# Optimization experiments

Hardware: AMD Instinct MI355X
Metric: run time of the kernel (lower is better)

Reference implementation:

```python
import jax, jax.numpy as jnp
import numpy as np

B, A, EMBED, HIDDEN, PROJ = 256, 16, 1024, 1024, 256


def setup_inputs() -> dict:
    key = jax.random.key(0)
    k0, k1, k2 = jax.random.split(key, 3)
    return {
        "agent_embeddings": jax.random.normal(k0, (B, A, EMBED), dtype=jnp.float32),
        "w1": jax.random.normal(k1, (EMBED, HIDDEN), dtype=jnp.float32) * (1.0 / np.sqrt(EMBED)),
        "b1": jnp.zeros((HIDDEN,), dtype=jnp.float32),
        "w2": jax.random.normal(k2, (HIDDEN, PROJ), dtype=jnp.float32) * (1.0 / np.sqrt(HIDDEN)),
        "b2": jnp.zeros((PROJ,), dtype=jnp.float32),
        "log_scale": jnp.asarray(0.0, dtype=jnp.float32),  # log(init_logit_scale=1.0)
        "logit_bias": jnp.asarray(0.0, dtype=jnp.float32),
    }


def reference(agent_embeddings, w1, b1, w2, b2, log_scale, logit_bias):
    b, a, d = agent_embeddings.shape
    n = b * a
    x = agent_embeddings.reshape(n, d)
    # MLP projector: Linear -> GELU (exact, torch default) -> [dropout=identity at eval] -> Linear
    h = jax.nn.gelu(x @ w1 + b1, approximate=False)
    p = h @ w2 + b2  # [N, proj_dim]
    z = p / jnp.linalg.norm(p, axis=-1, keepdims=True)
    # cosine similarity logits, scaled + biased
    logits = (z @ z.T) * jnp.exp(log_scale) + logit_bias  # [N, N]
    # block-diagonal labels: 1 iff same batch element
    ids = jnp.arange(n) // a
    m1 = jnp.where(ids[:, None] == ids[None, :], 1.0, -1.0)  # 2*labels - 1
    loglik = jax.nn.log_sigmoid(m1 * logits)
    loss = jnp.mean(-jnp.sum(loglik, axis=-1))
    embeddings = z.reshape(b, a, -1)
    return embeddings, loss, logits
```

## Files before the change

### kernel.cpp

```cpp
#include <hip/hip_runtime.h>
#include <math.h>


#define NTOK 4096
#define DEMB 1024
#define DHID 1024
#define DPRJ 256

typedef __attribute__((ext_vector_type(8))) short bf16x8;
typedef __attribute__((ext_vector_type(4))) float f32x4;

typedef __attribute__((address_space(3))) void lds_void_t;
typedef __attribute__((address_space(1))) const void gbl_void_t;

static __device__ __forceinline__ void glds16(const void* g, void* l) {
    __builtin_amdgcn_global_load_lds((gbl_void_t*)g, (lds_void_t*)l, 16, 0, 0);
}

static __device__ __forceinline__ void split2(float v, ushort* h, ushort* l) {
    const uint u = __float_as_uint(v);
    *h = (ushort)(u >> 16);
    const float r = v - __uint_as_float(u & 0xffff0000u);
    *l = (ushort)(__float_as_uint(r) >> 16);
}
static __device__ __forceinline__ float gelu_fast(float v) {
    const float x  = v * 0.70710678118654752440f;
    const float ax = fabsf(x);
    const float t  = 1.0f / (1.0f + 0.3275911f * ax);
    const float poly = t * (0.254829592f + t * (-0.284496736f + t * (1.421413741f
                     + t * (-1.453152027f + t * 1.061405429f))));
    const float erf_ax = 1.0f - poly * __expf(-ax * ax);
    return 0.5f * v * (1.0f + copysignf(erf_ax, x));
}
static __device__ __forceinline__ float log_sigmoid_fast(float x) {
    return fminf(x, 0.0f) - __logf(1.0f + __expf(-fabsf(x)));
}

__global__ __launch_bounds__(256)
void k_cvt_T(const float* __restrict__ W, ushort* __restrict__ WtH,
             ushort* __restrict__ WtL, int K, int N)
{
    __shared__ float tile[32][33];
    const int tn0 = blockIdx.x * 32;
    const int tk0 = blockIdx.y * 32;
    const int tr = threadIdx.x >> 5;
    const int tc = threadIdx.x & 31;
#pragma unroll
    for (int p = 0; p < 4; ++p)
        tile[tr + 8 * p][tc] = W[(size_t)(tk0 + tr + 8 * p) * N + tn0 + tc];
    __syncthreads();
#pragma unroll
    for (int p = 0; p < 4; ++p) {
        const int n = tr + 8 * p;
        ushort h, l;
        split2(tile[tc][n], &h, &l);
        WtH[(size_t)(tn0 + n) * K + tk0 + tc] = h;
        WtL[(size_t)(tn0 + n) * K + tk0 + tc] = l;
    }
}

#define G1_BUF 12288
__global__ __launch_bounds__(256, 3)
void k_gemm1(const float* __restrict__ X,
             const ushort* __restrict__ W1tH, const ushort* __restrict__ W1tL,
             const float* __restrict__ B1,
             ushort* __restrict__ Hh, ushort* __restrict__ Hl)
{
    __shared__ __align__(16) ushort sm[2 * G1_BUF];
    const int t = threadIdx.x, lane = t & 63, w = t >> 6;
    const int wr = w >> 1, wc = w & 1;
    const int bm = blockIdx.x * 128, bn = blockIdx.y * 64;
    const int kb = lane >> 4, lr = lane & 15;

    const int ar = t & 63;
    const float* xp0 = X + (size_t)(bm + ar) * DEMB + w * 8;
    const float* xp1 = xp0 + (size_t)64 * DEMB;
    const ushort* bhs = W1tH + (size_t)(bn + lane) * DEMB + w * 8;
    const ushort* bls = W1tL + (size_t)(bn + lane) * DEMB + w * 8;

    f32x4 acc[4][2];
#pragma unroll
    for (int i = 0; i < 4; ++i)
#pragma unroll
        for (int j = 0; j < 2; ++j) acc[i][j] = (f32x4){0.f, 0.f, 0.f, 0.f};

    {
        const float4 a00 = *(const float4*)(xp0);
        const float4 a01 = *(const float4*)(xp0 + 4);
        const float4 a10 = *(const float4*)(xp1);
        const float4 a11 = *(const float4*)(xp1 + 4);
        glds16(bhs, sm + 8192 + w * 512);
        glds16(bls, sm + 10240 + w * 512);
        const float va[8] = {a00.x, a00.y, a00.z, a00.w, a01.x, a01.y, a01.z, a01.w};
        const float vb[8] = {a10.x, a10.y, a10.z, a10.w, a11.x, a11.y, a11.z, a11.w};
        uint4 h0, l0, h1, l1;
#pragma unroll
        for (int e = 0; e < 8; ++e) {
            split2(va[e], (ushort*)&h0 + e, (ushort*)&l0 + e);
            split2(vb[e], (ushort*)&h1 + e, (ushort*)&l1 + e);
        }
        *(uint4*)(sm + w * 1024 + ar * 8)               = h0;
        *(uint4*)(sm + 4096 + w * 1024 + ar * 8)        = l0;
        *(uint4*)(sm + w * 1024 + (ar + 64) * 8)        = h1;
        *(uint4*)(sm + 4096 + w * 1024 + (ar + 64) * 8) = l1;
        __syncthreads();
    }

    int co = 0;
#pragma unroll 2
    for (int ks = 0; ks < 32; ++ks) {
        float4 a00, a01, a10, a11;
        if (ks < 31) {
            const int kt = (ks + 1) * 32;
            a00 = *(const float4*)(xp0 + kt);
            a01 = *(const float4*)(xp0 + kt + 4);
            a10 = *(const float4*)(xp1 + kt);
            a11 = *(const float4*)(xp1 + kt + 4);
            ushort* nb = sm + (co ^ G1_BUF);
            glds16(bhs + kt, nb + 8192 + w * 512);
            glds16(bls + kt, nb + 10240 + w * 512);
        }
        const ushort* cb = sm + co;
        bf16x8 bh[2], bl[2];
#pragma unroll
        for (int j = 0; j < 2; ++j) {
            const int o = kb * 512 + (wc * 32 + j * 16 + lr) * 8;
            bh[j] = *(const bf16x8*)(cb + 8192 + o);
            bl[j] = *(const bf16x8*)(cb + 10240 + o);
        }
#pragma unroll
        for (int i = 0; i < 4; ++i) {
            const int o = kb * 1024 + (wr * 64 + i * 16 + lr) * 8;
            const bf16x8 ah = *(const bf16x8*)(cb + o);
            const bf16x8 al = *(const bf16x8*)(cb + 4096 + o);
#pragma unroll
            for (int j = 0; j < 2; ++j) {
                acc[i][j] = __builtin_amdgcn_mfma_f32_16x16x32_bf16(ah, bh[j], acc[i][j], 0, 0, 0);
                acc[i][j] = __builtin_amdgcn_mfma_f32_16x16x32_bf16(ah, bl[j], acc[i][j], 0, 0, 0);
                acc[i][j] = __builtin_amdgcn_mfma_f32_16x16x32_bf16(al, bh[j], acc[i][j], 0, 0, 0);
            }
        }
        if (ks < 31) {
            ushort* nb = sm + (co ^ G1_BUF);
            const float va[8] = {a00.x, a00.y, a00.z, a00.w, a01.x, a01.y, a01.z, a01.w};
            const float vb[8] = {a10.x, a10.y, a10.z, a10.w, a11.x, a11.y, a11.z, a11.w};
            uint4 h0, l0, h1, l1;
#pragma unroll
            for (int e = 0; e < 8; ++e) {
                split2(va[e], (ushort*)&h0 + e, (ushort*)&l0 + e);
                split2(vb[e], (ushort*)&h1 + e, (ushort*)&l1 + e);
            }
            *(uint4*)(nb + w * 1024 + ar * 8)               = h0;
            *(uint4*)(nb + 4096 + w * 1024 + ar * 8)        = l0;
            *(uint4*)(nb + w * 1024 + (ar + 64) * 8)        = h1;
            *(uint4*)(nb + 4096 + w * 1024 + (ar + 64) * 8) = l1;
        }
        __syncthreads();
        co ^= G1_BUF;
    }

#pragma unroll
    for (int j = 0; j < 2; ++j) {
        const int col = bn + wc * 32 + j * 16 + lr;
        const float b = B1[col];
#pragma unroll
        for (int i = 0; i < 4; ++i) {
#pragma unroll
            for (int e = 0; e < 4; ++e) {
                const int row = bm + wr * 64 + i * 16 + kb * 4 + e;
                const float g = gelu_fast(acc[i][j][e] + b);
                ushort h, l;
                split2(g, &h, &l);
                Hh[(size_t)row * DHID + col] = h;
                Hl[(size_t)row * DHID + col] = l;
            }
        }
    }
}

#define G2_BUF 12288
__global__ __launch_bounds__(256, 3)
void k_gemm2(const ushort* __restrict__ Hh, const ushort* __restrict__ Hl,
             const ushort* __restrict__ W2tH, const ushort* __restrict__ W2tL,
             float* __restrict__ P)
{
    __shared__ __align__(16) ushort sm[2 * G2_BUF];
    const int t = threadIdx.x, lane = t & 63, w = t >> 6;
    const int wr = w >> 1, wc = w & 1;
    const int bm = blockIdx.x * 128, bn = blockIdx.y * 64;
    const int k0 = blockIdx.z * 512;
    const int kb = lane >> 4, lr = lane & 15;

    const ushort* ah0 = Hh + (size_t)(bm + lane) * DHID + k0 + w * 8;
    const ushort* ah1 = Hh + (size_t)(bm + 64 + lane) * DHID + k0 + w * 8;
    const ushort* al0 = Hl + (size_t)(bm + lane) * DHID + k0 + w * 8;
    const ushort* al1 = Hl + (size_t)(bm + 64 + lane) * DHID + k0 + w * 8;
    const ushort* bhs = W2tH + (size_t)(bn + lane) * DHID + k0 + w * 8;
    const ushort* bls = W2tL + (size_t)(bn + lane) * DHID + k0 + w * 8;

    f32x4 acc[4][2];
#pragma unroll
    for (int i = 0; i < 4; ++i)
#pragma unroll
        for (int j = 0; j < 2; ++j) acc[i][j] = (f32x4){0.f, 0.f, 0.f, 0.f};

#define G2_STAGE(buf, kt)                                   \
    glds16(ah0 + (kt), (buf) + w * 1024);                   \
    glds16(ah1 + (kt), (buf) + w * 1024 + 512);             \
    glds16(al0 + (kt), (buf) + 4096 + w * 1024);            \
    glds16(al1 + (kt), (buf) + 4096 + w * 1024 + 512);      \
    glds16(bhs + (kt), (buf) + 8192 + w * 512);             \
    glds16(bls + (kt), (buf) + 10240 + w * 512);

    { G2_STAGE(sm, 0); __syncthreads(); }

    int co = 0;
#pragma unroll 2
    for (int ks = 0; ks < 16; ++ks) {
        if (ks < 15) {
            ushort* nb = sm + (co ^ G2_BUF);
            const int kt = (ks + 1) * 32;
            G2_STAGE(nb, kt);
        }
        const ushort* cb = sm + co;
        bf16x8 bh[2], bl[2];
#pragma unroll
        for (int j = 0; j < 2; ++j) {
            const int o = kb * 512 + (wc * 32 + j * 16 + lr) * 8;
            bh[j] = *(const bf16x8*)(cb + 8192 + o);
            bl[j] = *(const bf16x8*)(cb + 10240 + o);
        }
#pragma unroll
        for (int i = 0; i < 4; ++i) {
            const int o = kb * 1024 + (wr * 64 + i * 16 + lr) * 8;
            const bf16x8 ah = *(const bf16x8*)(cb + o);
            const bf16x8 al = *(const bf16x8*)(cb + 4096 + o);
#pragma unroll
            for (int j = 0; j < 2; ++j) {
                acc[i][j] = __builtin_amdgcn_mfma_f32_16x16x32_bf16(ah, bh[j], acc[i][j], 0, 0, 0);
                acc[i][j] = __builtin_amdgcn_mfma_f32_16x16x32_bf16(ah, bl[j], acc[i][j], 0, 0, 0);
                acc[i][j] = __builtin_amdgcn_mfma_f32_16x16x32_bf16(al, bh[j], acc[i][j], 0, 0, 0);
            }
        }
        __syncthreads();
        co ^= G2_BUF;
    }

    float* Pz = P + (size_t)blockIdx.z * NTOK * DPRJ;
#pragma unroll
    for (int j = 0; j < 2; ++j) {
        const int col = bn + wc * 32 + j * 16 + lr;
#pragma unroll
        for (int i = 0; i < 4; ++i) {
#pragma unroll
            for (int e = 0; e < 4; ++e) {
                const int row = bm + wr * 64 + i * 16 + kb * 4 + e;
                Pz[(size_t)row * DPRJ + col] = acc[i][j][e];
            }
        }
    }
}

__global__ __launch_bounds__(256)
void k_norm(const float* __restrict__ P, const float* __restrict__ B2,
            float* __restrict__ Zo, ushort* __restrict__ Zbh,
            ushort* __restrict__ Zbl)
{
    const int r = blockIdx.x;
    const int c = threadIdx.x;

    const float v = P[(size_t)r * DPRJ + c]
                  + P[(size_t)NTOK * DPRJ + (size_t)r * DPRJ + c] + B2[c];
    float ss = v * v;
#pragma unroll
    for (int o = 32; o > 0; o >>= 1) ss += __shfl_down(ss, o);
    __shared__ float wsum[4];
    if ((c & 63) == 0) wsum[c >> 6] = ss;
    __syncthreads();
    const float tot = wsum[0] + wsum[1] + wsum[2] + wsum[3];
    const float z = v / sqrtf(tot);
    Zo[(size_t)r * DPRJ + c] = z;
    ushort h, l;
    split2(z, &h, &l);
    Zbh[(size_t)r * DPRJ + c] = h;
    Zbl[(size_t)r * DPRJ + c] = l;
}

#define G3_BUF 16384
__global__ __launch_bounds__(256, 2)
void k_gemm3(const ushort* __restrict__ Zbh, const ushort* __restrict__ Zbl,
             const float* __restrict__ LS, const float* __restrict__ LB,
             float* __restrict__ Lg, float* __restrict__ partial)
{
    __shared__ __align__(16) ushort sm[2 * G3_BUF];
    const int t = threadIdx.x, lane = t & 63, w = t >> 6;
    const int wr = w >> 1, wc = w & 1;
    const int bm = blockIdx.x * 128, bn = blockIdx.y * 128;
    const int kb = lane >> 4, lr = lane & 15;

    const ushort* aH0 = Zbh + (size_t)(bm + lane) * DPRJ + w * 8;
    const ushort* aH1 = Zbh + (size_t)(bm + 64 + lane) * DPRJ + w * 8;
    const ushort* aL0 = Zbl + (size_t)(bm + lane) * DPRJ + w * 8;
    const ushort* aL1 = Zbl + (size_t)(bm + 64 + lane) * DPRJ + w * 8;
    const ushort* bH0 = Zbh + (size_t)(bn + lane) * DPRJ + w * 8;
    const ushort* bH1 = Zbh + (size_t)(bn + 64 + lane) * DPRJ + w * 8;
    const ushort* bL0 = Zbl + (size_t)(bn + lane) * DPRJ + w * 8;
    const ushort* bL1 = Zbl + (size_t)(bn + 64 + lane) * DPRJ + w * 8;

    f32x4 acc[4][4];
#pragma unroll
    for (int i = 0; i < 4; ++i)
#pragma unroll
        for (int j = 0; j < 4; ++j) acc[i][j] = (f32x4){0.f, 0.f, 0.f, 0.f};

#define G3_STAGE(buf, kt)                                    \
    glds16(aH0 + (kt), (buf) + w * 1024);                    \
    glds16(aH1 + (kt), (buf) + w * 1024 + 512);              \
    glds16(aL0 + (kt), (buf) + 4096 + w * 1024);             \
    glds16(aL1 + (kt), (buf) + 4096 + w * 1024 + 512);       \
    glds16(bH0 + (kt), (buf) + 8192 + w * 1024);             \
    glds16(bH1 + (kt), (buf) + 8192 + w * 1024 + 512);       \
    glds16(bL0 + (kt), (buf) + 12288 + w * 1024);            \
    glds16(bL1 + (kt), (buf) + 12288 + w * 1024 + 512);

    { G3_STAGE(sm, 0); __syncthreads(); }

    int co = 0;
#pragma unroll
    for (int ks = 0; ks < 8; ++ks) {
        if (ks < 7) {
            ushort* nb = sm + (co ^ G3_BUF);
            const int kt = (ks + 1) * 32;
            G3_STAGE(nb, kt);
        }
        const ushort* cb = sm + co;
        bf16x8 bh[4], bl[4];
#pragma unroll
        for (int j = 0; j < 4; ++j) {
            const int o = kb * 1024 + (wc * 64 + j * 16 + lr) * 8;
            bh[j] = *(const bf16x8*)(cb + 8192 + o);
            bl[j] = *(const bf16x8*)(cb + 12288 + o);
        }
#pragma unroll
        for (int i = 0; i < 4; ++i) {
            const int o = kb * 1024 + (wr * 64 + i * 16 + lr) * 8;
            const bf16x8 ah = *(const bf16x8*)(cb + o);
            const bf16x8 al = *(const bf16x8*)(cb + 4096 + o);
#pragma unroll
            for (int j = 0; j < 4; ++j) {
                acc[i][j] = __builtin_amdgcn_mfma_f32_16x16x32_bf16(ah, bh[j], acc[i][j], 0, 0, 0);
                acc[i][j] = __builtin_amdgcn_mfma_f32_16x16x32_bf16(ah, bl[j], acc[i][j], 0, 0, 0);
                acc[i][j] = __builtin_amdgcn_mfma_f32_16x16x32_bf16(al, bh[j], acc[i][j], 0, 0, 0);
            }
        }
        __syncthreads();
        co ^= G3_BUF;
    }

    const float scale = __expf(LS[0]);
    const float lbias = LB[0];
    float lsum = 0.0f;
#pragma unroll
    for (int j = 0; j < 4; ++j) {
        const int col = bn + wc * 64 + j * 16 + lr;
        const int cid = col >> 4;
#pragma unroll
        for (int i = 0; i < 4; ++i) {
#pragma unroll
            for (int e = 0; e < 4; ++e) {
                const int row = bm + wr * 64 + i * 16 + kb * 4 + e;
                const float lg = fmaf(acc[i][j][e], scale, lbias);
                Lg[(size_t)row * NTOK + col] = lg;
                const float x = ((row >> 4) == cid) ? lg : -lg;
                lsum += log_sigmoid_fast(x);
            }
        }
    }

#pragma unroll
    for (int o = 32; o > 0; o >>= 1) lsum += __shfl_down(lsum, o);
    __shared__ float wsum[4];
    if ((t & 63) == 0) wsum[t >> 6] = lsum;
    __syncthreads();
    if (t == 0)
        partial[blockIdx.y * gridDim.x + blockIdx.x]
            = wsum[0] + wsum[1] + wsum[2] + wsum[3];
}

__global__ __launch_bounds__(256)
void k_finalize(const float* __restrict__ partial, float* __restrict__ loss_out)
{
    const int t = threadIdx.x;
    double s = (double)partial[t] + (double)partial[t + 256]
             + (double)partial[t + 512] + (double)partial[t + 768];
#pragma unroll
    for (int o = 32; o > 0; o >>= 1) s += __shfl_down(s, o);
    __shared__ double ws4[4];
    if ((t & 63) == 0) ws4[t >> 6] = s;
    __syncthreads();
    if (t == 0)
        loss_out[0] = (float)(-(ws4[0] + ws4[1] + ws4[2] + ws4[3]) / (double)NTOK);
}

extern "C" void kernel_launch(void* const* d_in, const int* in_sizes, int n_in,
                              void* d_out, int out_size, void* d_ws, size_t ws_size,
                              hipStream_t stream)
{
    const float* X  = (const float*)d_in[0];
    const float* W1 = (const float*)d_in[1];
    const float* B1 = (const float*)d_in[2];
    const float* W2 = (const float*)d_in[3];
    const float* B2 = (const float*)d_in[4];
    const float* LS = (const float*)d_in[5];
    const float* LB = (const float*)d_in[6];

    float* out  = (float*)d_out;
    float* Zo   = out;
    float* loss = out + (size_t)NTOK * DPRJ;
    float* Lg   = loss + 1;

    char* ws = (char*)d_ws;
    ushort* Hh   = (ushort*)(ws);
    ushort* Hl   = (ushort*)(ws + 8388608);
    ushort* W1tH = (ushort*)(ws + 16777216);
    ushort* W1tL = (ushort*)(ws + 18874368);
    float*  P    = (float*) (ws + 16777216);
    ushort* W2tH = (ushort*)(ws + 25165824);
    ushort* W2tL = (ushort*)(ws + 25690112);
    ushort* Zbh  = (ushort*)(ws + 26214400);
    ushort* Zbl  = (ushort*)(ws + 28311552);
    float*  part = (float*) (ws + 30408704);

    k_cvt_T <<<dim3(32, 32),    256, 0, stream>>>(W1, W1tH, W1tL, DEMB, DHID);
    k_cvt_T <<<dim3(8, 32),     256, 0, stream>>>(W2, W2tH, W2tL, DHID, DPRJ);
    k_gemm1 <<<dim3(32, 16),    256, 0, stream>>>(X, W1tH, W1tL, B1, Hh, Hl);
    k_gemm2 <<<dim3(32, 4, 2),  256, 0, stream>>>(Hh, Hl, W2tH, W2tL, P);
    k_norm  <<<dim3(4096),      256, 0, stream>>>(P, B2, Zo, Zbh, Zbl);
    k_gemm3 <<<dim3(32, 32),    256, 0, stream>>>(Zbh, Zbl, LS, LB, Lg, part);
    k_finalize<<<1, 256, 0, stream>>>(part, loss);
}
```

Before: 231.2 us.

## Restructure logits GEMM: 512 threads, XOR-swizzled half-K LDS tiles, coalesced store

Rewrites the z·zᵀ logits kernel to use 8 waves per block, each computing a 64x32 sub-tile. Operands are staged in two large K-phases of 128 with an XOR-swizzled LDS layout to avoid bank conflicts, replacing the 8-step double buffer. Results are staged through LDS so the 64 MB logits matrix is written with fully coalesced row stores. The cost is a 128 KB LDS footprint, which limits occupancy to one block per CU, and load/compute overlap across phases is lost.

```diff
diff --git a/kernel.cpp b/kernel.cpp
--- a/kernel.cpp
+++ b/kernel.cpp
@@ -286,105 +286,119 @@
     Zbl[(size_t)r * DPRJ + c] = l;
 }
 
-#define G3_BUF 16384
-__global__ __launch_bounds__(256, 2)
+__global__ __launch_bounds__(512, 1)
 void k_gemm3(const ushort* __restrict__ Zbh, const ushort* __restrict__ Zbl,
              const float* __restrict__ LS, const float* __restrict__ LB,
              float* __restrict__ Lg, float* __restrict__ partial)
 {
-    __shared__ __align__(16) ushort sm[2 * G3_BUF];
+    __shared__ __align__(16) ushort sm[65536];
+    ushort* Ah = sm;
+    ushort* Al = sm + 16384;
+    ushort* Bh = sm + 32768;
+    ushort* Bl = sm + 49152;
+
     const int t = threadIdx.x, lane = t & 63, w = t >> 6;
-    const int wr = w >> 1, wc = w & 1;
+    const int wr = w >> 2, wc = w & 3;
     const int bm = blockIdx.x * 128, bn = blockIdx.y * 128;
     const int kb = lane >> 4, lr = lane & 15;
 
-    const ushort* aH0 = Zbh + (size_t)(bm + lane) * DPRJ + w * 8;
-    const ushort* aH1 = Zbh + (size_t)(bm + 64 + lane) * DPRJ + w * 8;
-    const ushort* aL0 = Zbl + (size_t)(bm + lane) * DPRJ + w * 8;
-    const ushort* aL1 = Zbl + (size_t)(bm + 64 + lane) * DPRJ + w * 8;
-    const ushort* bH0 = Zbh + (size_t)(bn + lane) * DPRJ + w * 8;
-    const ushort* bH1 = Zbh + (size_t)(bn + 64 + lane) * DPRJ + w * 8;
-    const ushort* bL0 = Zbl + (size_t)(bn + lane) * DPRJ + w * 8;
-    const ushort* bL1 = Zbl + (size_t)(bn + 64 + lane) * DPRJ + w * 8;
-
-    f32x4 acc[4][4];
+    const int srow0 = w * 16;
+
+    f32x4 acc[4][2];
 #pragma unroll
     for (int i = 0; i < 4; ++i)
 #pragma unroll
-        for (int j = 0; j < 4; ++j) acc[i][j] = (f32x4){0.f, 0.f, 0.f, 0.f};
-
-#define G3_STAGE(buf, kt)                                    \
-    glds16(aH0 + (kt), (buf) + w * 1024);                    \
-    glds16(aH1 + (kt), (buf) + w * 1024 + 512);              \
-    glds16(aL0 + (kt), (buf) + 4096 + w * 1024);             \
-    glds16(aL1 + (kt), (buf) + 4096 + w * 1024 + 512);       \
-    glds16(bH0 + (kt), (buf) + 8192 + w * 1024);             \
-    glds16(bH1 + (kt), (buf) + 8192 + w * 1024 + 512);       \
-    glds16(bL0 + (kt), (buf) + 12288 + w * 1024);            \
-    glds16(bL1 + (kt), (buf) + 12288 + w * 1024 + 512);
-
-    { G3_STAGE(sm, 0); __syncthreads(); }
-
-    int co = 0;
-#pragma unroll
-    for (int ks = 0; ks < 8; ++ks) {
-        if (ks < 7) {
-            ushort* nb = sm + (co ^ G3_BUF);
-            const int kt = (ks + 1) * 32;
-            G3_STAGE(nb, kt);
-        }
-        const ushort* cb = sm + co;
-        bf16x8 bh[4], bl[4];
-#pragma unroll
-        for (int j = 0; j < 4; ++j) {
-            const int o = kb * 1024 + (wc * 64 + j * 16 + lr) * 8;
-            bh[j] = *(const bf16x8*)(cb + 8192 + o);
-            bl[j] = *(const bf16x8*)(cb + 12288 + o);
-        }
-#pragma unroll
-        for (int i = 0; i < 4; ++i) {
-            const int o = kb * 1024 + (wr * 64 + i * 16 + lr) * 8;
-            const bf16x8 ah = *(const bf16x8*)(cb + o);
-            const bf16x8 al = *(const bf16x8*)(cb + 4096 + o);
-#pragma unroll
-            for (int j = 0; j < 4; ++j) {
-                acc[i][j] = __builtin_amdgcn_mfma_f32_16x16x32_bf16(ah, bh[j], acc[i][j], 0, 0, 0);
-                acc[i][j] = __builtin_amdgcn_mfma_f32_16x16x32_bf16(ah, bl[j], acc[i][j], 0, 0, 0);
-                acc[i][j] = __builtin_amdgcn_mfma_f32_16x16x32_bf16(al, bh[j], acc[i][j], 0, 0, 0);
-            }
+        for (int j = 0; j < 2; ++j) acc[i][j] = (f32x4){0.f, 0.f, 0.f, 0.f};
+
+    float lsum = 0.0f;
+
+#pragma unroll
+    for (int ph = 0; ph < 2; ++ph) {
+        const int ko = ph * 128;
+        if (ph) __syncthreads();
+
+#pragma unroll
+        for (int q = 0; q < 4; ++q) {
+            const int row = srow0 + q * 4 + (lane >> 4);
+            const int gck = (lane & 15) ^ (row & 15);
+            const size_t ga = (size_t)(bm + row) * DPRJ + ko + (gck << 3);
+            const size_t gb = (size_t)(bn + row) * DPRJ + ko + (gck << 3);
+            const int lo = (srow0 + q * 4) * 128;
+            glds16(Zbh + ga, Ah + lo);
+            glds16(Zbl + ga, Al + lo);
+            glds16(Zbh + gb, Bh + lo);
+            glds16(Zbl + gb, Bl + lo);
         }
         __syncthreads();
-        co ^= G3_BUF;
+
+#pragma unroll
+        for (int ks = 0; ks < 4; ++ks) {
+            const int g = ks * 4 + kb;
+            bf16x8 bhf[2], blf[2];
+#pragma unroll
+            for (int j = 0; j < 2; ++j) {
+                const int col = wc * 32 + j * 16 + lr;
+                const int o = col * 128 + ((g ^ (col & 15)) << 3);
+                bhf[j] = *(const bf16x8*)(Bh + o);
+                blf[j] = *(const bf16x8*)(Bl + o);
+            }
+#pragma unroll
+            for (int i = 0; i < 4; ++i) {
+                const int row = wr * 64 + i * 16 + lr;
+                const int o = row * 128 + ((g ^ (row & 15)) << 3);
+                const bf16x8 ah = *(const bf16x8*)(Ah + o);
+                const bf16x8 al = *(const bf16x8*)(Al + o);
+#pragma unroll
+                for (int j = 0; j < 2; ++j) {
+                    acc[i][j] = __builtin_amdgcn_mfma_f32_16x16x32_bf16(ah, bhf[j], acc[i][j], 0, 0, 0);
+                    acc[i][j] = __builtin_amdgcn_mfma_f32_16x16x32_bf16(ah, blf[j], acc[i][j], 0, 0, 0);
+                    acc[i][j] = __builtin_amdgcn_mfma_f32_16x16x32_bf16(al, bhf[j], acc[i][j], 0, 0, 0);
+                }
+            }
+        }
     }
 
     const float scale = __expf(LS[0]);
     const float lbias = LB[0];
-    float lsum = 0.0f;
-#pragma unroll
-    for (int j = 0; j < 4; ++j) {
-        const int col = bn + wc * 64 + j * 16 + lr;
+
+    __syncthreads();
+    float* fT = (float*)sm;
+#pragma unroll
+    for (int j = 0; j < 2; ++j) {
+        const int col = bn + wc * 32 + j * 16 + lr;
         const int cid = col >> 4;
 #pragma unroll
         for (int i = 0; i < 4; ++i) {
 #pragma unroll
             for (int e = 0; e < 4; ++e) {
-                const int row = bm + wr * 64 + i * 16 + kb * 4 + e;
+                const int rloc = wr * 64 + i * 16 + kb * 4 + e;
                 const float lg = fmaf(acc[i][j][e], scale, lbias);
-                Lg[(size_t)row * NTOK + col] = lg;
-                const float x = ((row >> 4) == cid) ? lg : -lg;
+                fT[rloc * 132 + (wc * 32 + j * 16 + lr)] = lg;
+                const float x = (((bm + rloc) >> 4) == cid) ? lg : -lg;
                 lsum += log_sigmoid_fast(x);
             }
         }
     }
+    __syncthreads();
+
+#pragma unroll
+    for (int q = 0; q < 32; ++q) {
+        const int e = q * 512 + t;
+        const int row = e >> 7, c = e & 127;
+        Lg[(size_t)(bm + row) * NTOK + bn + c] = fT[row * 132 + c];
+    }
 
 #pragma unroll
     for (int o = 32; o > 0; o >>= 1) lsum += __shfl_down(lsum, o);
-    __shared__ float wsum[4];
-    if ((t & 63) == 0) wsum[t >> 6] = lsum;
-    __syncthreads();
-    if (t == 0)
-        partial[blockIdx.y * gridDim.x + blockIdx.x]
-            = wsum[0] + wsum[1] + wsum[2] + wsum[3];
+    __shared__ float wsum[8];
+    if (lane == 0) wsum[w] = lsum;
+    __syncthreads();
+    if (t == 0) {
+        float s = 0.f;
+#pragma unroll
+        for (int i = 0; i < 8; ++i) s += wsum[i];
+        partial[blockIdx.y * gridDim.x + blockIdx.x] = s;
+    }
 }
 
 __global__ __launch_bounds__(256)
@@ -436,6 +450,6 @@
     k_gemm1 <<<dim3(32, 16),    256, 0, stream>>>(X, W1tH, W1tL, B1, Hh, Hl);
     k_gemm2 <<<dim3(32, 4, 2),  256, 0, stream>>>(Hh, Hl, W2tH, W2tL, P);
     k_norm  <<<dim3(4096),      256, 0, stream>>>(P, B2, Zo, Zbh, Zbl);
-    k_gemm3 <<<dim3(32, 32),    256, 0, stream>>>(Zbh, Zbl, LS, LB, Lg, part);
+    k_gemm3 <<<dim3(32, 32),    512, 0, stream>>>(Zbh, Zbl, LS, LB, Lg, part);
     k_finalize<<<1, 256, 0, stream>>>(part, loss);
 }
```

After: 223.1 us. 3.5% less time.
